# Performance work log

Hardware: AMD Instinct MI355X
Metric: run time of the kernel (lower is better)

The kernel has to match this reference:

```python
import jax, jax.numpy as jnp
import numpy as np

N_NODES = 20000
N_EDGES = 320000
N_GRAPHS = 128


def gat_conv(x, W, attn_l, attn_r, bias, src, dst, num_nodes):
    """DGL-style GATConv: per-edge attention, edge softmax over incoming
    edges of each destination node, scatter-sum aggregation."""
    H, D = attn_l.shape
    feat = (x @ W).reshape(-1, H, D)                      # [N,H,D]
    el = jnp.sum(feat * attn_l, axis=-1)                  # [N,H]
    er = jnp.sum(feat * attn_r, axis=-1)                  # [N,H]
    e = jax.nn.leaky_relu(el[src] + er[dst], 0.2)         # [E,H]
    # numerically stable segment softmax over dst
    m = jax.ops.segment_max(e, dst, num_segments=num_nodes)   # [N,H]
    e_exp = jnp.exp(e - m[dst])                               # [E,H]
    denom = jax.ops.segment_sum(e_exp, dst, num_segments=num_nodes)
    alpha = e_exp / denom[dst]                                 # [E,H]
    msg = alpha[:, :, None] * feat[src]                        # [E,H,D]
    rst = jax.ops.segment_sum(msg, dst, num_segments=num_nodes)  # [N,H,D]
    return rst + bias.reshape(1, H, D)


def setup_inputs() -> dict:
    key = jax.random.key(0)
    ks = jax.random.split(key, 12)
    s1 = 1.0 / np.sqrt(256.0)
    s2 = 1.0 / np.sqrt(512.0)
    return {
        "x": jax.random.normal(ks[0], (N_NODES, 256), dtype=jnp.float32),
        "W1": jax.random.normal(ks[1], (256, 512), dtype=jnp.float32) * s1,
        "a_l1": jax.random.normal(ks[2], (8, 64), dtype=jnp.float32) * 0.1,
        "a_r1": jax.random.normal(ks[3], (8, 64), dtype=jnp.float32) * 0.1,
        "b1": jnp.zeros((512,), dtype=jnp.float32),
        "W2": jax.random.normal(ks[4], (512, 128), dtype=jnp.float32) * s2,
        "a_l2": jax.random.normal(ks[5], (1, 128), dtype=jnp.float32) * 0.1,
        "a_r2": jax.random.normal(ks[6], (1, 128), dtype=jnp.float32) * 0.1,
        "b2": jnp.zeros((128,), dtype=jnp.float32),
        "edge_src": jax.random.randint(ks[7], (N_EDGES,), 0, N_NODES, dtype=jnp.int32),
        "edge_dst": jax.random.randint(ks[8], (N_EDGES,), 0, N_NODES, dtype=jnp.int32),
        "graph_ids": jnp.sort(jax.random.randint(ks[9], (N_NODES,), 0, N_GRAPHS, dtype=jnp.int32)),
    }


def reference(x, W1, a_l1, a_r1, b1, W2, a_l2, a_r2, b2, edge_src, edge_dst, graph_ids):
    h = gat_conv(x, W1, a_l1, a_r1, b1, edge_src, edge_dst, N_NODES)  # [N,8,64]
    h = h.reshape(N_NODES, -1)                                        # flatten(1)
    h = gat_conv(h, W2, a_l2, a_r2, b2, edge_src, edge_dst, N_NODES)  # [N,1,128]
    # dgl.mean_nodes: per-graph mean pooling
    ones = jnp.ones((N_NODES,), dtype=h.dtype)
    counts = jax.ops.segment_sum(ones, graph_ids, num_segments=N_GRAPHS)
    sums = jax.ops.segment_sum(h, graph_ids, num_segments=N_GRAPHS)   # [G,1,128]
    hg = sums / jnp.maximum(counts, 1.0)[:, None, None]
    return hg
```

## Files before the change

kernel.cpp:

```cpp
#include <hip/hip_runtime.h>
#include <hip/hip_fp16.h>

#define N_NODES  20000
#define N_EDGES  320000
#define N_GRAPHS 128

typedef _Float16 half8 __attribute__((ext_vector_type(8)));
typedef float    f32x4 __attribute__((ext_vector_type(4)));

__global__ void fill_zero(int* __restrict__ p, int n) {
    int i = blockIdx.x * blockDim.x + threadIdx.x;
    int stride = gridDim.x * blockDim.x;
    for (; i < n; i += stride) p[i] = 0;
}

__global__ void setup_misc(const float* __restrict__ W1, const float* __restrict__ W2,
                           __half* __restrict__ w1t, __half* __restrict__ w2t,
                           const int* __restrict__ gid, int* __restrict__ gstart) {
    int i = blockIdx.x * blockDim.x + threadIdx.x;
    if (i < 256 * 512) {
        int r = i >> 9, c = i & 511;
        w1t[c * 256 + r] = __float2half(W1[i]);
    } else if (i < 256 * 512 + 512 * 128) {
        int j = i - 256 * 512;
        int r = j >> 7, c = j & 127;
        w2t[c * 512 + r] = __float2half(W2[j]);
    } else {
        int g = i - (256 * 512 + 512 * 128);
        if (g <= N_GRAPHS) {
            if (g == N_GRAPHS) { gstart[N_GRAPHS] = N_NODES; return; }
            int lo = 0, hi = N_NODES;
            while (lo < hi) {
                int mid = (lo + hi) >> 1;
                if (gid[mid] < g) lo = mid + 1; else hi = mid;
            }
            gstart[g] = lo;
        }
    }
}

template <int BM, int BN, int WM, int WN, int H, int D, bool AF32>
__global__ __launch_bounds__(256) void gemm_mfma(
        const void* __restrict__ A_, const __half* __restrict__ BT,
        __half* __restrict__ C, const float* __restrict__ al,
        const float* __restrict__ ar, float* __restrict__ el,
        float* __restrict__ er, int Mm, int Nn, int Kk) {
    constexpr int BK  = 32;
    constexpr int MFR = WM / 16, NFR = WN / 16;
    constexpr int WCOLS = BN / WN;
    __shared__ __align__(16) __half As[BM * BK];
    __shared__ __align__(16) __half Bs[BN * BK];
    const int tid  = threadIdx.x;
    const int w    = tid >> 6, lane = tid & 63;
    const int wr   = w / WCOLS, wc = w % WCOLS;
    const int brow = blockIdx.x * BM;
    const int bcol = blockIdx.y * BN;
    const int lr   = lane & 15;
    const int lk   = (lane >> 4) * 8;

    f32x4 acc[MFR][NFR] = {};

    for (int k0 = 0; k0 < Kk; k0 += BK) {
        for (int c = tid; c < BM * 4; c += 256) {
            int r = c >> 2, ko = (c & 3) * 8;
            int gr = brow + r; if (gr >= Mm) gr = Mm - 1;
            int off = (r * BK + ko) ^ ((r & 7) << 3);
            if constexpr (AF32) {
                const float* ap = (const float*)A_ + (size_t)gr * Kk + k0 + ko;
                float4 v0 = *reinterpret_cast<const float4*>(ap);
                float4 v1 = *reinterpret_cast<const float4*>(ap + 4);
                union { __half2 h2[4]; uint4 u; } pk;
                pk.h2[0] = __floats2half2_rn(v0.x, v0.y);
                pk.h2[1] = __floats2half2_rn(v0.z, v0.w);
                pk.h2[2] = __floats2half2_rn(v1.x, v1.y);
                pk.h2[3] = __floats2half2_rn(v1.z, v1.w);
                *reinterpret_cast<uint4*>(&As[off]) = pk.u;
            } else {
                *reinterpret_cast<uint4*>(&As[off]) =
                    *reinterpret_cast<const uint4*>((const __half*)A_ + (size_t)gr * Kk + k0 + ko);
            }
        }
        for (int c = tid; c < BN * 4; c += 256) {
            int r = c >> 2, ko = (c & 3) * 8;
            int off = (r * BK + ko) ^ ((r & 7) << 3);
            *reinterpret_cast<uint4*>(&Bs[off]) =
                *reinterpret_cast<const uint4*>(&BT[(size_t)(bcol + r) * Kk + k0 + ko]);
        }
        __syncthreads();
        half8 af[MFR], bf[NFR];
#pragma unroll
        for (int m = 0; m < MFR; ++m) {
            int r = wr * WM + m * 16 + lr;
            af[m] = *reinterpret_cast<const half8*>(&As[(r * BK + lk) ^ ((r & 7) << 3)]);
        }
#pragma unroll
        for (int n = 0; n < NFR; ++n) {
            int r = wc * WN + n * 16 + lr;
            bf[n] = *reinterpret_cast<const half8*>(&Bs[(r * BK + lk) ^ ((r & 7) << 3)]);
        }
#pragma unroll
        for (int m = 0; m < MFR; ++m)
#pragma unroll
            for (int n = 0; n < NFR; ++n)
                acc[m][n] = __builtin_amdgcn_mfma_f32_16x16x32_f16(af[m], bf[n], acc[m][n], 0, 0, 0);
        __syncthreads();
    }

#pragma unroll
    for (int m = 0; m < MFR; ++m) {
        int r0 = brow + wr * WM + m * 16 + ((lane >> 4) << 2);
#pragma unroll
        for (int n = 0; n < NFR; ++n) {
            int cc = bcol + wc * WN + n * 16 + lr;
#pragma unroll
            for (int g = 0; g < 4; ++g)
                if (r0 + g < Mm) C[(size_t)(r0 + g) * Nn + cc] = __float2half(acc[m][n][g]);
        }
    }
    const int h = (bcol + wc * WN) / D;
    float alv[NFR], arv[NFR];
#pragma unroll
    for (int n = 0; n < NFR; ++n) {
        alv[n] = al[bcol + wc * WN + n * 16 + lr];
        arv[n] = ar[bcol + wc * WN + n * 16 + lr];
    }
#pragma unroll
    for (int m = 0; m < MFR; ++m) {
#pragma unroll
        for (int g = 0; g < 4; ++g) {
            float pl = 0.f, pr = 0.f;
#pragma unroll
            for (int n = 0; n < NFR; ++n) {
                pl += acc[m][n][g] * alv[n];
                pr += acc[m][n][g] * arv[n];
            }
            pl += __shfl_xor(pl, 1); pl += __shfl_xor(pl, 2);
            pl += __shfl_xor(pl, 4); pl += __shfl_xor(pl, 8);
            pr += __shfl_xor(pr, 1); pr += __shfl_xor(pr, 2);
            pr += __shfl_xor(pr, 4); pr += __shfl_xor(pr, 8);
            int gr = brow + wr * WM + m * 16 + ((lane >> 4) << 2) + g;
            if (lr == 0 && gr < Mm) {
                if constexpr (WN == D) {
                    el[(size_t)gr * H + h] = pl;
                    er[(size_t)gr * H + h] = pr;
                } else {
                    atomicAdd(&el[(size_t)gr * H + h], pl);
                    atomicAdd(&er[(size_t)gr * H + h], pr);
                }
            }
        }
    }
}

__global__ void hist_kernel(const int* __restrict__ dst, int* __restrict__ deg, int E) {
    int e = blockIdx.x * blockDim.x + threadIdx.x;
    if (e >= E) return;
    atomicAdd(&deg[dst[e]], 1);
}

__global__ void scan_kernel(const int* __restrict__ deg, int* __restrict__ rowptr, int n) {
    __shared__ int partial[1024];
    const int t = threadIdx.x;
    const int CH = (n + 1023) / 1024;
    const int base = t * CH;
    int local = 0;
    for (int i = 0; i < CH; ++i)
        if (base + i < n) local += deg[base + i];
    partial[t] = local;
    __syncthreads();
    for (int o = 1; o < 1024; o <<= 1) {
        int v = (t >= o) ? partial[t - o] : 0;
        __syncthreads();
        partial[t] += v;
        __syncthreads();
    }
    int run = (t == 0) ? 0 : partial[t - 1];
    for (int i = 0; i < CH; ++i) {
        if (base + i <= n) rowptr[base + i] = run;
        if (base + i < n) run += deg[base + i];
    }
}

__global__ void scatter_kernel(const int* __restrict__ src, const int* __restrict__ dst,
                               const int* __restrict__ rowptr, int* __restrict__ cursor,
                               int* __restrict__ esrc, int E) {
    int e = blockIdx.x * blockDim.x + threadIdx.x;
    if (e >= E) return;
    int d = dst[e];
    int pos = rowptr[d] + atomicAdd(&cursor[d], 1);
    esrc[pos] = src[e];
}

template <int F, int H, bool HOUT>
__global__ __launch_bounds__(256) void node_aggr_wave(
        const __half* __restrict__ feat, const float* __restrict__ el,
        const float* __restrict__ er, const int* __restrict__ rowptr,
        const int* __restrict__ esrc, const float* __restrict__ bias,
        void* __restrict__ rst_, int N) {
    constexpr int LPN = F / 8;
    constexpr int NPW = 64 / LPN;
    constexpr int D   = F / H;
    const int wid  = (blockIdx.x * blockDim.x + threadIdx.x) >> 6;
    const int lane = threadIdx.x & 63;
    const int n    = wid * NPW + lane / LPN;
    if (n >= N) return;
    const int col = (lane % LPN) * 8;
    const int h   = col / D;
    const float ern = er[(size_t)n * H + h];
    const int rs = rowptr[n], re = rowptr[n + 1];
    const __half* fq = feat + col;

    float acc[8] = {};
    float dsum = 0.f;
    int i = rs;
    for (; i + 4 <= re; i += 4) {
        int s0 = esrc[i], s1 = esrc[i + 1], s2 = esrc[i + 2], s3 = esrc[i + 3];
        float x0 = el[(size_t)s0 * H + h] + ern;
        float x1 = el[(size_t)s1 * H + h] + ern;
        float x2 = el[(size_t)s2 * H + h] + ern;
        float x3 = el[(size_t)s3 * H + h] + ern;
        x0 = (x0 > 0.f) ? x0 : 0.2f * x0;
        x1 = (x1 > 0.f) ? x1 : 0.2f * x1;
        x2 = (x2 > 0.f) ? x2 : 0.2f * x2;
        x3 = (x3 > 0.f) ? x3 : 0.2f * x3;
        float w0 = __expf(x0), w1 = __expf(x1), w2 = __expf(x2), w3 = __expf(x3);
        union { uint4 u; __half2 h2[4]; } r0, r1, r2, r3;
        r0.u = *reinterpret_cast<const uint4*>(fq + (size_t)s0 * F);
        r1.u = *reinterpret_cast<const uint4*>(fq + (size_t)s1 * F);
        r2.u = *reinterpret_cast<const uint4*>(fq + (size_t)s2 * F);
        r3.u = *reinterpret_cast<const uint4*>(fq + (size_t)s3 * F);
        dsum += (w0 + w1) + (w2 + w3);
#pragma unroll
        for (int k = 0; k < 4; ++k) {
            float2 f0 = __half22float2(r0.h2[k]);
            float2 f1 = __half22float2(r1.h2[k]);
            float2 f2 = __half22float2(r2.h2[k]);
            float2 f3 = __half22float2(r3.h2[k]);
            acc[2 * k]     += w0 * f0.x + w1 * f1.x + w2 * f2.x + w3 * f3.x;
            acc[2 * k + 1] += w0 * f0.y + w1 * f1.y + w2 * f2.y + w3 * f3.y;
        }
    }
    for (; i < re; ++i) {
        int s = esrc[i];
        float x = el[(size_t)s * H + h] + ern;
        x = (x > 0.f) ? x : 0.2f * x;
        float w = __expf(x);
        union { uint4 u; __half2 h2[4]; } r;
        r.u = *reinterpret_cast<const uint4*>(fq + (size_t)s * F);
        dsum += w;
#pragma unroll
        for (int k = 0; k < 4; ++k) {
            float2 f = __half22float2(r.h2[k]);
            acc[2 * k]     += w * f.x;
            acc[2 * k + 1] += w * f.y;
        }
    }
    float inv = (re > rs) ? 1.f / dsum : 0.f;
    float4 b0 = *reinterpret_cast<const float4*>(bias + col);
    float4 b1 = *reinterpret_cast<const float4*>(bias + col + 4);
    float o[8] = {acc[0] * inv + b0.x, acc[1] * inv + b0.y,
                  acc[2] * inv + b0.z, acc[3] * inv + b0.w,
                  acc[4] * inv + b1.x, acc[5] * inv + b1.y,
                  acc[6] * inv + b1.z, acc[7] * inv + b1.w};
    if constexpr (HOUT) {
        union { __half2 h2[4]; uint4 u; } pk;
        pk.h2[0] = __floats2half2_rn(o[0], o[1]);
        pk.h2[1] = __floats2half2_rn(o[2], o[3]);
        pk.h2[2] = __floats2half2_rn(o[4], o[5]);
        pk.h2[3] = __floats2half2_rn(o[6], o[7]);
        *reinterpret_cast<uint4*>((__half*)rst_ + (size_t)n * F + col) = pk.u;
    } else {
        float* op = (float*)rst_ + (size_t)n * F + col;
        *reinterpret_cast<float4*>(op)     = make_float4(o[0], o[1], o[2], o[3]);
        *reinterpret_cast<float4*>(op + 4) = make_float4(o[4], o[5], o[6], o[7]);
    }
}

__global__ __launch_bounds__(1024) void seg_pool_kernel(
        const float* __restrict__ h, const int* __restrict__ start,
        float* __restrict__ out, int D) {
    __shared__ float part[7][128];
    int g = blockIdx.x;
    int d = threadIdx.x & 127;
    int j = threadIdx.x >> 7;
    int s = start[g], e = start[g + 1];
    float acc = 0.f;
    for (int n = s + j; n < e; n += 8) acc += h[(size_t)n * D + d];
    if (j > 0) part[j - 1][d] = acc;
    __syncthreads();
    if (j == 0) {
#pragma unroll
        for (int k = 0; k < 7; ++k) acc += part[k][d];
        out[(size_t)g * D + d] = acc / fmaxf((float)(e - s), 1.f);
    }
}

extern "C" void kernel_launch(void* const* d_in, const int* in_sizes, int n_in,
                              void* d_out, int out_size, void* d_ws, size_t ws_size,
                              hipStream_t stream) {
    const float* x   = (const float*)d_in[0];
    const float* W1  = (const float*)d_in[1];
    const float* al1 = (const float*)d_in[2];
    const float* ar1 = (const float*)d_in[3];
    const float* b1  = (const float*)d_in[4];
    const float* W2  = (const float*)d_in[5];
    const float* al2 = (const float*)d_in[6];
    const float* ar2 = (const float*)d_in[7];
    const float* b2  = (const float*)d_in[8];
    const int* src   = (const int*)d_in[9];
    const int* dst   = (const int*)d_in[10];
    const int* gid   = (const int*)d_in[11];
    float* out = (float*)d_out;

    float* ws = (float*)d_ws;
    size_t off = 0;
    int* deg    = (int*)(ws + off); off += N_NODES;
    int* cursor = (int*)(ws + off); off += N_NODES;
    const size_t zeroN = off;
    int* rowptr = (int*)(ws + off); off += N_NODES + 4;
    int* gstart = (int*)(ws + off); off += N_GRAPHS + 4;
    int* esrc   = (int*)(ws + off); off += N_EDGES;
    __half* w1t    = (__half*)(ws + off); off += 512 * 256 / 2;
    __half* w2t    = (__half*)(ws + off); off += 128 * 512 / 2;
    __half* feat1h = (__half*)(ws + off); off += (size_t)N_NODES * 256;
    float*  el1    = ws + off; off += (size_t)N_NODES * 8;
    float*  er1    = ws + off; off += (size_t)N_NODES * 8;
    __half* rst1h  = (__half*)(ws + off); off += (size_t)N_NODES * 256;
    __half* feat2h = (__half*)(ws + off); off += (size_t)N_NODES * 64;
    float*  el2    = ws + off; off += N_NODES;
    float*  er2    = ws + off; off += N_NODES;
    float*  rst2   = ws + off; off += (size_t)N_NODES * 128;

    fill_zero<<<40, 256, 0, stream>>>((int*)ws, (int)zeroN);

    hist_kernel<<<(N_EDGES + 255) / 256, 256, 0, stream>>>(dst, deg, N_EDGES);
    scan_kernel<<<1, 1024, 0, stream>>>(deg, rowptr, N_NODES);
    scatter_kernel<<<(N_EDGES + 255) / 256, 256, 0, stream>>>(src, dst, rowptr, cursor, esrc, N_EDGES);
    setup_misc<<<(256 * 512 + 512 * 128 + N_GRAPHS + 1 + 255) / 256, 256, 0, stream>>>(
        W1, W2, w1t, w2t, gid, gstart);

    dim3 g1((N_NODES + 127) / 128, 512 / 128);
    gemm_mfma<128, 128, 64, 64, 8, 64, true><<<g1, 256, 0, stream>>>(
        x, w1t, feat1h, al1, ar1, el1, er1, N_NODES, 512, 256);
    node_aggr_wave<512, 8, true><<<(N_NODES * 64 + 255) / 256, 256, 0, stream>>>(
        feat1h, el1, er1, rowptr, esrc, b1, rst1h, N_NODES);

    dim3 g2((N_NODES + 63) / 64, 128 / 128);
    gemm_mfma<64, 128, 16, 128, 1, 128, false><<<g2, 256, 0, stream>>>(
        rst1h, w2t, feat2h, al2, ar2, el2, er2, N_NODES, 128, 512);
    node_aggr_wave<128, 1, false><<<(N_NODES * 16 + 255) / 256, 256, 0, stream>>>(
        feat2h, el2, er2, rowptr, esrc, b2, rst2, N_NODES);

    seg_pool_kernel<<<N_GRAPHS, 1024, 0, stream>>>(rst2, gstart, out, 128);
}
```

Baseline: 198.0 us.

## Merge CSR build and weight prep into one cooperative prologue kernel

Replaces five setup launches (zero-fill, histogram, scan, scatter, weight transpose) with one cooperative kernel that uses grid-wide syncs between phases. It also converts x to fp16 up front so the first GEMM reads half-precision input instead of converting fp32 tiles on the fly. The aim is to cut launch gaps and redundant per-tile conversion. The cost is grid.sync overhead, a single-block scan with 256 threads instead of 1024, and an extra x write and read pass.

```diff
diff --git a/kernel.cpp b/kernel.cpp
--- a/kernel.cpp
+++ b/kernel.cpp
@@ -1,5 +1,8 @@
 #include <hip/hip_runtime.h>
 #include <hip/hip_fp16.h>
+#include <hip/hip_cooperative_groups.h>
+
+namespace cg = cooperative_groups;
 
 #define N_NODES  20000
 #define N_EDGES  320000
@@ -8,40 +11,83 @@
 typedef _Float16 half8 __attribute__((ext_vector_type(8)));
 typedef float    f32x4 __attribute__((ext_vector_type(4)));
 
-__global__ void fill_zero(int* __restrict__ p, int n) {
-    int i = blockIdx.x * blockDim.x + threadIdx.x;
-    int stride = gridDim.x * blockDim.x;
-    for (; i < n; i += stride) p[i] = 0;
-}
-
-__global__ void setup_misc(const float* __restrict__ W1, const float* __restrict__ W2,
-                           __half* __restrict__ w1t, __half* __restrict__ w2t,
-                           const int* __restrict__ gid, int* __restrict__ gstart) {
-    int i = blockIdx.x * blockDim.x + threadIdx.x;
-    if (i < 256 * 512) {
+__global__ void prologue(const float* __restrict__ W1, const float* __restrict__ W2,
+                         __half* __restrict__ w1t, __half* __restrict__ w2t,
+                         const int* __restrict__ gid, int* __restrict__ gstart,
+                         const float* __restrict__ x, __half* __restrict__ xh,
+                         const int* __restrict__ src, const int* __restrict__ dst,
+                         int* __restrict__ deg, int* __restrict__ cursor,
+                         int* __restrict__ rowptr, int* __restrict__ esrc) {
+    cg::grid_group grid = cg::this_grid();
+    const int tid  = blockIdx.x * blockDim.x + threadIdx.x;
+    const int nthr = gridDim.x * blockDim.x;
+
+    for (int i = tid; i < N_NODES; i += nthr) { deg[i] = 0; cursor[i] = 0; }
+    for (int i = tid; i < 256 * 512; i += nthr) {
         int r = i >> 9, c = i & 511;
         w1t[c * 256 + r] = __float2half(W1[i]);
-    } else if (i < 256 * 512 + 512 * 128) {
-        int j = i - 256 * 512;
-        int r = j >> 7, c = j & 127;
-        w2t[c * 512 + r] = __float2half(W2[j]);
-    } else {
-        int g = i - (256 * 512 + 512 * 128);
-        if (g <= N_GRAPHS) {
-            if (g == N_GRAPHS) { gstart[N_GRAPHS] = N_NODES; return; }
+    }
+    for (int i = tid; i < 512 * 128; i += nthr) {
+        int r = i >> 7, c = i & 127;
+        w2t[c * 512 + r] = __float2half(W2[i]);
+    }
+    if (tid <= N_GRAPHS) {
+        if (tid == N_GRAPHS) gstart[N_GRAPHS] = N_NODES;
+        else {
             int lo = 0, hi = N_NODES;
             while (lo < hi) {
                 int mid = (lo + hi) >> 1;
-                if (gid[mid] < g) lo = mid + 1; else hi = mid;
+                if (gid[mid] < tid) lo = mid + 1; else hi = mid;
             }
-            gstart[g] = lo;
-        }
-    }
-}
-
-template <int BM, int BN, int WM, int WN, int H, int D, bool AF32>
+            gstart[tid] = lo;
+        }
+    }
+    for (int i = tid; i < N_NODES * 64; i += nthr) {
+        float4 v = *reinterpret_cast<const float4*>(&x[(size_t)i * 4]);
+        union { __half2 h2[2]; uint2 u; } pk;
+        pk.h2[0] = __floats2half2_rn(v.x, v.y);
+        pk.h2[1] = __floats2half2_rn(v.z, v.w);
+        *reinterpret_cast<uint2*>(&xh[(size_t)i * 4]) = pk.u;
+    }
+    grid.sync();
+
+    for (int e = tid; e < N_EDGES; e += nthr) atomicAdd(&deg[dst[e]], 1);
+    grid.sync();
+
+    if (blockIdx.x == 0) {
+        __shared__ int partial[256];
+        const int t = threadIdx.x;
+        const int CH = (N_NODES + 255) / 256;
+        const int base = t * CH;
+        int local = 0;
+        for (int i = 0; i < CH; ++i)
+            if (base + i < N_NODES) local += deg[base + i];
+        partial[t] = local;
+        __syncthreads();
+        for (int o = 1; o < 256; o <<= 1) {
+            int v = (t >= o) ? partial[t - o] : 0;
+            __syncthreads();
+            partial[t] += v;
+            __syncthreads();
+        }
+        int run = (t == 0) ? 0 : partial[t - 1];
+        for (int i = 0; i < CH; ++i) {
+            if (base + i <= N_NODES) rowptr[base + i] = run;
+            if (base + i < N_NODES) run += deg[base + i];
+        }
+    }
+    grid.sync();
+
+    for (int e = tid; e < N_EDGES; e += nthr) {
+        int d = dst[e];
+        int pos = rowptr[d] + atomicAdd(&cursor[d], 1);
+        esrc[pos] = src[e];
+    }
+}
+
+template <int BM, int BN, int WM, int WN, int H, int D>
 __global__ __launch_bounds__(256) void gemm_mfma(
-        const void* __restrict__ A_, const __half* __restrict__ BT,
+        const __half* __restrict__ A, const __half* __restrict__ BT,
         __half* __restrict__ C, const float* __restrict__ al,
         const float* __restrict__ ar, float* __restrict__ el,
         float* __restrict__ er, int Mm, int Nn, int Kk) {
@@ -65,20 +111,8 @@
             int r = c >> 2, ko = (c & 3) * 8;
             int gr = brow + r; if (gr >= Mm) gr = Mm - 1;
             int off = (r * BK + ko) ^ ((r & 7) << 3);
-            if constexpr (AF32) {
-                const float* ap = (const float*)A_ + (size_t)gr * Kk + k0 + ko;
-                float4 v0 = *reinterpret_cast<const float4*>(ap);
-                float4 v1 = *reinterpret_cast<const float4*>(ap + 4);
-                union { __half2 h2[4]; uint4 u; } pk;
-                pk.h2[0] = __floats2half2_rn(v0.x, v0.y);
-                pk.h2[1] = __floats2half2_rn(v0.z, v0.w);
-                pk.h2[2] = __floats2half2_rn(v1.x, v1.y);
-                pk.h2[3] = __floats2half2_rn(v1.z, v1.w);
-                *reinterpret_cast<uint4*>(&As[off]) = pk.u;
-            } else {
-                *reinterpret_cast<uint4*>(&As[off]) =
-                    *reinterpret_cast<const uint4*>((const __half*)A_ + (size_t)gr * Kk + k0 + ko);
-            }
+            *reinterpret_cast<uint4*>(&As[off]) =
+                *reinterpret_cast<const uint4*>(&A[(size_t)gr * Kk + k0 + ko]);
         }
         for (int c = tid; c < BN * 4; c += 256) {
             int r = c >> 2, ko = (c & 3) * 8;
@@ -150,45 +184,6 @@
             }
         }
     }
-}
-
-__global__ void hist_kernel(const int* __restrict__ dst, int* __restrict__ deg, int E) {
-    int e = blockIdx.x * blockDim.x + threadIdx.x;
-    if (e >= E) return;
-    atomicAdd(&deg[dst[e]], 1);
-}
-
-__global__ void scan_kernel(const int* __restrict__ deg, int* __restrict__ rowptr, int n) {
-    __shared__ int partial[1024];
-    const int t = threadIdx.x;
-    const int CH = (n + 1023) / 1024;
-    const int base = t * CH;
-    int local = 0;
-    for (int i = 0; i < CH; ++i)
-        if (base + i < n) local += deg[base + i];
-    partial[t] = local;
-    __syncthreads();
-    for (int o = 1; o < 1024; o <<= 1) {
-        int v = (t >= o) ? partial[t - o] : 0;
-        __syncthreads();
-        partial[t] += v;
-        __syncthreads();
-    }
-    int run = (t == 0) ? 0 : partial[t - 1];
-    for (int i = 0; i < CH; ++i) {
-        if (base + i <= n) rowptr[base + i] = run;
-        if (base + i < n) run += deg[base + i];
-    }
-}
-
-__global__ void scatter_kernel(const int* __restrict__ src, const int* __restrict__ dst,
-                               const int* __restrict__ rowptr, int* __restrict__ cursor,
-                               int* __restrict__ esrc, int E) {
-    int e = blockIdx.x * blockDim.x + threadIdx.x;
-    if (e >= E) return;
-    int d = dst[e];
-    int pos = rowptr[d] + atomicAdd(&cursor[d], 1);
-    esrc[pos] = src[e];
 }
 
 template <int F, int H, bool HOUT>
@@ -316,10 +311,10 @@
     size_t off = 0;
     int* deg    = (int*)(ws + off); off += N_NODES;
     int* cursor = (int*)(ws + off); off += N_NODES;
-    const size_t zeroN = off;
     int* rowptr = (int*)(ws + off); off += N_NODES + 4;
     int* gstart = (int*)(ws + off); off += N_GRAPHS + 4;
     int* esrc   = (int*)(ws + off); off += N_EDGES;
+    __half* xh     = (__half*)(ws + off); off += (size_t)N_NODES * 128;
     __half* w1t    = (__half*)(ws + off); off += 512 * 256 / 2;
     __half* w2t    = (__half*)(ws + off); off += 128 * 512 / 2;
     __half* feat1h = (__half*)(ws + off); off += (size_t)N_NODES * 256;
@@ -331,22 +326,25 @@
     float*  er2    = ws + off; off += N_NODES;
     float*  rst2   = ws + off; off += (size_t)N_NODES * 128;
 
-    fill_zero<<<40, 256, 0, stream>>>((int*)ws, (int)zeroN);
-
-    hist_kernel<<<(N_EDGES + 255) / 256, 256, 0, stream>>>(dst, deg, N_EDGES);
-    scan_kernel<<<1, 1024, 0, stream>>>(deg, rowptr, N_NODES);
-    scatter_kernel<<<(N_EDGES + 255) / 256, 256, 0, stream>>>(src, dst, rowptr, cursor, esrc, N_EDGES);
-    setup_misc<<<(256 * 512 + 512 * 128 + N_GRAPHS + 1 + 255) / 256, 256, 0, stream>>>(
-        W1, W2, w1t, w2t, gid, gstart);
+    {
+        void* args[] = {
+            (void*)&W1, (void*)&W2, (void*)&w1t, (void*)&w2t,
+            (void*)&gid, (void*)&gstart, (void*)&x, (void*)&xh,
+            (void*)&src, (void*)&dst, (void*)&deg, (void*)&cursor,
+            (void*)&rowptr, (void*)&esrc
+        };
+        hipLaunchCooperativeKernel((void*)prologue, dim3(1024), dim3(256),
+                                   args, 0, stream);
+    }
 
     dim3 g1((N_NODES + 127) / 128, 512 / 128);
-    gemm_mfma<128, 128, 64, 64, 8, 64, true><<<g1, 256, 0, stream>>>(
-        x, w1t, feat1h, al1, ar1, el1, er1, N_NODES, 512, 256);
+    gemm_mfma<128, 128, 64, 64, 8, 64><<<g1, 256, 0, stream>>>(
+        xh, w1t, feat1h, al1, ar1, el1, er1, N_NODES, 512, 256);
     node_aggr_wave<512, 8, true><<<(N_NODES * 64 + 255) / 256, 256, 0, stream>>>(
         feat1h, el1, er1, rowptr, esrc, b1, rst1h, N_NODES);
 
     dim3 g2((N_NODES + 63) / 64, 128 / 128);
-    gemm_mfma<64, 128, 16, 128, 1, 128, false><<<g2, 256, 0, stream>>>(
+    gemm_mfma<64, 128, 16, 128, 1, 128><<<g2, 256, 0, stream>>>(
         rst1h, w2t, feat2h, al2, ar2, el2, er2, N_NODES, 128, 512);
     node_aggr_wave<128, 1, false><<<(N_NODES * 16 + 255) / 256, 256, 0, stream>>>(
         feat2h, el2, er2, rowptr, esrc, b2, rst2, N_NODES);
```

After: 510.9 us. 158% more time.

## Fuse setup kernels and overlap CSR scatter with first GEMM launch

Applied to the files above, without the earlier changes.

Merges weight transposition, graph-start search and degree histogram into one grid-stride kernel. The CSR edge scatter now runs as extra blocks inside the first GEMM launch, and the zero-fill kernel becomes a memset. The aim is to cut kernel launch count and let scatter work overlap with the GEMM. The cost is a heterogeneous launch where block mapping changes from a 2D grid to a linearized index, and the GEMM's el/er atomics path is unchanged.

```diff
diff --git a/kernel.cpp b/kernel.cpp
--- a/kernel.cpp
+++ b/kernel.cpp
@@ -8,39 +8,60 @@
 typedef _Float16 half8 __attribute__((ext_vector_type(8)));
 typedef float    f32x4 __attribute__((ext_vector_type(4)));
 
-__global__ void fill_zero(int* __restrict__ p, int n) {
-    int i = blockIdx.x * blockDim.x + threadIdx.x;
-    int stride = gridDim.x * blockDim.x;
-    for (; i < n; i += stride) p[i] = 0;
-}
-
-__global__ void setup_misc(const float* __restrict__ W1, const float* __restrict__ W2,
+__global__ void setup_hist(const float* __restrict__ W1, const float* __restrict__ W2,
                            __half* __restrict__ w1t, __half* __restrict__ w2t,
-                           const int* __restrict__ gid, int* __restrict__ gstart) {
-    int i = blockIdx.x * blockDim.x + threadIdx.x;
-    if (i < 256 * 512) {
+                           const int* __restrict__ gid, int* __restrict__ gstart,
+                           const int* __restrict__ dst, int* __restrict__ deg) {
+    const int tid  = blockIdx.x * blockDim.x + threadIdx.x;
+    const int nthr = gridDim.x * blockDim.x;
+    for (int i = tid; i < 256 * 512; i += nthr) {
         int r = i >> 9, c = i & 511;
         w1t[c * 256 + r] = __float2half(W1[i]);
-    } else if (i < 256 * 512 + 512 * 128) {
-        int j = i - 256 * 512;
-        int r = j >> 7, c = j & 127;
-        w2t[c * 512 + r] = __float2half(W2[j]);
-    } else {
-        int g = i - (256 * 512 + 512 * 128);
-        if (g <= N_GRAPHS) {
-            if (g == N_GRAPHS) { gstart[N_GRAPHS] = N_NODES; return; }
+    }
+    for (int i = tid; i < 512 * 128; i += nthr) {
+        int r = i >> 7, c = i & 127;
+        w2t[c * 512 + r] = __float2half(W2[i]);
+    }
+    if (tid <= N_GRAPHS) {
+        if (tid == N_GRAPHS) gstart[N_GRAPHS] = N_NODES;
+        else {
             int lo = 0, hi = N_NODES;
             while (lo < hi) {
                 int mid = (lo + hi) >> 1;
-                if (gid[mid] < g) lo = mid + 1; else hi = mid;
+                if (gid[mid] < tid) lo = mid + 1; else hi = mid;
             }
-            gstart[g] = lo;
-        }
+            gstart[tid] = lo;
+        }
+    }
+    for (int e = tid; e < N_EDGES; e += nthr) atomicAdd(&deg[dst[e]], 1);
+}
+
+__global__ void scan_kernel(const int* __restrict__ deg, int* __restrict__ rowptr, int n) {
+    __shared__ int partial[1024];
+    const int t = threadIdx.x;
+    const int CH = (n + 1023) / 1024;
+    const int base = t * CH;
+    int local = 0;
+    for (int i = 0; i < CH; ++i)
+        if (base + i < n) local += deg[base + i];
+    partial[t] = local;
+    __syncthreads();
+    for (int o = 1; o < 1024; o <<= 1) {
+        int v = (t >= o) ? partial[t - o] : 0;
+        __syncthreads();
+        partial[t] += v;
+        __syncthreads();
+    }
+    int run = (t == 0) ? 0 : partial[t - 1];
+    for (int i = 0; i < CH; ++i) {
+        if (base + i <= n) rowptr[base + i] = run;
+        if (base + i < n) run += deg[base + i];
     }
 }
 
 template <int BM, int BN, int WM, int WN, int H, int D, bool AF32>
-__global__ __launch_bounds__(256) void gemm_mfma(
+__device__ __forceinline__ void gemm_body(
+        int bx, int by,
         const void* __restrict__ A_, const __half* __restrict__ BT,
         __half* __restrict__ C, const float* __restrict__ al,
         const float* __restrict__ ar, float* __restrict__ el,
@@ -53,8 +74,8 @@
     const int tid  = threadIdx.x;
     const int w    = tid >> 6, lane = tid & 63;
     const int wr   = w / WCOLS, wc = w % WCOLS;
-    const int brow = blockIdx.x * BM;
-    const int bcol = blockIdx.y * BN;
+    const int brow = bx * BM;
+    const int bcol = by * BN;
     const int lr   = lane & 15;
     const int lk   = (lane >> 4) * 8;
 
@@ -152,43 +173,37 @@
     }
 }
 
-__global__ void hist_kernel(const int* __restrict__ dst, int* __restrict__ deg, int E) {
-    int e = blockIdx.x * blockDim.x + threadIdx.x;
-    if (e >= E) return;
-    atomicAdd(&deg[dst[e]], 1);
-}
-
-__global__ void scan_kernel(const int* __restrict__ deg, int* __restrict__ rowptr, int n) {
-    __shared__ int partial[1024];
-    const int t = threadIdx.x;
-    const int CH = (n + 1023) / 1024;
-    const int base = t * CH;
-    int local = 0;
-    for (int i = 0; i < CH; ++i)
-        if (base + i < n) local += deg[base + i];
-    partial[t] = local;
-    __syncthreads();
-    for (int o = 1; o < 1024; o <<= 1) {
-        int v = (t >= o) ? partial[t - o] : 0;
-        __syncthreads();
-        partial[t] += v;
-        __syncthreads();
-    }
-    int run = (t == 0) ? 0 : partial[t - 1];
-    for (int i = 0; i < CH; ++i) {
-        if (base + i <= n) rowptr[base + i] = run;
-        if (base + i < n) run += deg[base + i];
-    }
-}
-
-__global__ void scatter_kernel(const int* __restrict__ src, const int* __restrict__ dst,
-                               const int* __restrict__ rowptr, int* __restrict__ cursor,
-                               int* __restrict__ esrc, int E) {
-    int e = blockIdx.x * blockDim.x + threadIdx.x;
-    if (e >= E) return;
-    int d = dst[e];
-    int pos = rowptr[d] + atomicAdd(&cursor[d], 1);
-    esrc[pos] = src[e];
+template <int BM, int BN, int WM, int WN, int H, int D, bool AF32>
+__global__ __launch_bounds__(256) void gemm_kernel(
+        const void* __restrict__ A_, const __half* __restrict__ BT,
+        __half* __restrict__ C, const float* __restrict__ al,
+        const float* __restrict__ ar, float* __restrict__ el,
+        float* __restrict__ er, int Mm, int Nn, int Kk) {
+    gemm_body<BM, BN, WM, WN, H, D, AF32>(blockIdx.x, blockIdx.y, A_, BT, C,
+                                          al, ar, el, er, Mm, Nn, Kk);
+}
+
+template <int BM, int BN, int WM, int WN, int H, int D, bool AF32>
+__global__ __launch_bounds__(256) void gemm_scatter_kernel(
+        const void* __restrict__ A_, const __half* __restrict__ BT,
+        __half* __restrict__ C, const float* __restrict__ al,
+        const float* __restrict__ ar, float* __restrict__ el,
+        float* __restrict__ er, int Mm, int Nn, int Kk, int gemmRows,
+        const int* __restrict__ src, const int* __restrict__ dst,
+        const int* __restrict__ rowptr, int* __restrict__ cursor,
+        int* __restrict__ esrc) {
+    const int nbGemm = gemmRows * (Nn / BN);
+    if ((int)blockIdx.x < nbGemm) {
+        gemm_body<BM, BN, WM, WN, H, D, AF32>(blockIdx.x % gemmRows, blockIdx.x / gemmRows,
+                                              A_, BT, C, al, ar, el, er, Mm, Nn, Kk);
+    } else {
+        int e = (blockIdx.x - nbGemm) * blockDim.x + threadIdx.x;
+        if (e < N_EDGES) {
+            int d = dst[e];
+            int pos = rowptr[d] + atomicAdd(&cursor[d], 1);
+            esrc[pos] = src[e];
+        }
+    }
 }
 
 template <int F, int H, bool HOUT>
@@ -316,7 +331,6 @@
     size_t off = 0;
     int* deg    = (int*)(ws + off); off += N_NODES;
     int* cursor = (int*)(ws + off); off += N_NODES;
-    const size_t zeroN = off;
     int* rowptr = (int*)(ws + off); off += N_NODES + 4;
     int* gstart = (int*)(ws + off); off += N_GRAPHS + 4;
     int* esrc   = (int*)(ws + off); off += N_EDGES;
@@ -331,22 +345,23 @@
     float*  er2    = ws + off; off += N_NODES;
     float*  rst2   = ws + off; off += (size_t)N_NODES * 128;
 
-    fill_zero<<<40, 256, 0, stream>>>((int*)ws, (int)zeroN);
-
-    hist_kernel<<<(N_EDGES + 255) / 256, 256, 0, stream>>>(dst, deg, N_EDGES);
+    hipMemsetAsync(deg, 0, sizeof(int) * 2 * N_NODES, stream);
+
+    setup_hist<<<(N_EDGES + 255) / 256, 256, 0, stream>>>(
+        W1, W2, w1t, w2t, gid, gstart, dst, deg);
     scan_kernel<<<1, 1024, 0, stream>>>(deg, rowptr, N_NODES);
-    scatter_kernel<<<(N_EDGES + 255) / 256, 256, 0, stream>>>(src, dst, rowptr, cursor, esrc, N_EDGES);
-    setup_misc<<<(256 * 512 + 512 * 128 + N_GRAPHS + 1 + 255) / 256, 256, 0, stream>>>(
-        W1, W2, w1t, w2t, gid, gstart);
-
-    dim3 g1((N_NODES + 127) / 128, 512 / 128);
-    gemm_mfma<128, 128, 64, 64, 8, 64, true><<<g1, 256, 0, stream>>>(
-        x, w1t, feat1h, al1, ar1, el1, er1, N_NODES, 512, 256);
+
+    const int g1rows = (N_NODES + 127) / 128;
+    const int g1nb   = g1rows * (512 / 128);
+    const int scb    = (N_EDGES + 255) / 256;
+    gemm_scatter_kernel<128, 128, 64, 64, 8, 64, true><<<g1nb + scb, 256, 0, stream>>>(
+        x, w1t, feat1h, al1, ar1, el1, er1, N_NODES, 512, 256, g1rows,
+        src, dst, rowptr, cursor, esrc);
     node_aggr_wave<512, 8, true><<<(N_NODES * 64 + 255) / 256, 256, 0, stream>>>(
         feat1h, el1, er1, rowptr, esrc, b1, rst1h, N_NODES);
 
-    dim3 g2((N_NODES + 63) / 64, 128 / 128);
-    gemm_mfma<64, 128, 16, 128, 1, 128, false><<<g2, 256, 0, stream>>>(
+    dim3 g2((N_NODES + 63) / 64, 1);
+    gemm_kernel<64, 128, 16, 128, 1, 128, false><<<g2, 256, 0, stream>>>(
         rst1h, w2t, feat2h, al2, ar2, el2, er2, N_NODES, 128, 512);
     node_aggr_wave<128, 1, false><<<(N_NODES * 16 + 255) / 256, 256, 0, stream>>>(
         feat2h, el2, er2, rowptr, esrc, b2, rst2, N_NODES);
```

New measurement: 181.8 us. 8.2% less time.
